# Optimization experiments

Measured on AMD Instinct MI355X. Metric: run time of the kernel, lower is better.

The kernel has to match this reference:

```python
import jax, jax.numpy as jnp
import numpy as np

NEG_SLOPE = 0.01  # torch nn.LeakyReLU default


def setup_inputs() -> dict:
    key = jax.random.key(0)
    k1, k2, k3 = jax.random.split(key, 3)
    B, H, D, L = 4, 8, 64, 2048
    q = jax.random.normal(k1, (B, H, D, L), dtype=jnp.float32)
    k = jax.random.normal(k2, (B, H, D, L), dtype=jnp.float32)
    v = jax.random.normal(k3, (B, H, D, L), dtype=jnp.float32)
    return {"q": q, "k": k, "v": v}


def reference(q, k, v):
    # q, k, v: [B, H, D, L] (note: feature dim BEFORE length, as in the torch module)
    d_tensor = q.shape[2]
    scale = 1.0 / np.sqrt(d_tensor).astype(np.float32)
    # scores = LeakyReLU(q^T k / sqrt(d)) : [B, H, Lq, Lk]
    scores = jnp.einsum('bhdq,bhdk->bhqk', q, k) * scale
    scores = jax.nn.leaky_relu(scores, negative_slope=NEG_SLOPE)
    psi = jax.nn.softmax(scores, axis=-1)
    # out = (psi @ v^T)^T : [B, H, D, Lq]
    out = jnp.einsum('bhqk,bhdk->bhdq', psi, v)
    return out
```

## Files before the change

kernel.cpp:

```cpp
#include <hip/hip_runtime.h>
#include <math.h>

#define DD 64
#define LL 2048
#define TQ 128
#define TK 64
#define NT 512
#define SCALE_LOG2 (0.125f * 1.44269504088896340736f)

typedef __bf16 bf16_t;
typedef __bf16 bf16x8 __attribute__((ext_vector_type(8)));
typedef __bf16 bf16x4 __attribute__((ext_vector_type(4)));
typedef float f32x4 __attribute__((ext_vector_type(4)));

union __align__(16) SMem {
  struct {
    bf16_t Qs[TQ][72];
    bf16_t Ks[TK][72];
    bf16_t Vs[DD][72];
    bf16_t Ps[TQ][72];
  } a;
  float Oe[TQ][65];
};

__device__ __forceinline__ unsigned pack_bf16(float lo, float hi) {
  union { bf16_t b[2]; unsigned u; } p;
  p.b[0] = (bf16_t)lo; p.b[1] = (bf16_t)hi;
  return p.u;
}

__global__ __launch_bounds__(512, 4)
void attn_flash_bf16(const float* __restrict__ q, const float* __restrict__ k,
                     const float* __restrict__ v, float* __restrict__ out) {
  __shared__ SMem sm;
  const int tid  = threadIdx.x;
  const int w    = tid >> 6;
  const int lane = tid & 63;
  const int qu   = lane >> 4;
  const int c    = lane & 15;
  const int head = blockIdx.y;
  const int q0   = blockIdx.x * TQ;
  const size_t hoff = (size_t)head * DD * LL;
  const float* qp = q + hoff;
  const float* kp = k + hoff;
  const float* vp = v + hoff;

  for (int i = 0; i < 2; ++i) {
    int idx = tid + NT * i;
    int d2  = idx >> 5;
    int c4  = (idx & 31) * 4;
    float4 qa = *(const float4*)(qp + (2 * d2) * LL + q0 + c4);
    float4 qb = *(const float4*)(qp + (2 * d2 + 1) * LL + q0 + c4);
    *(unsigned*)&sm.a.Qs[c4 + 0][2 * d2] = pack_bf16(qa.x, qb.x);
    *(unsigned*)&sm.a.Qs[c4 + 1][2 * d2] = pack_bf16(qa.y, qb.y);
    *(unsigned*)&sm.a.Qs[c4 + 2][2 * d2] = pack_bf16(qa.z, qb.z);
    *(unsigned*)&sm.a.Qs[c4 + 3][2 * d2] = pack_bf16(qa.w, qb.w);
  }
  __syncthreads();

  bf16x8 aq[2];
  aq[0] = *(const bf16x8*)&sm.a.Qs[w * 16 + c][qu * 8];
  aq[1] = *(const bf16x8*)&sm.a.Qs[w * 16 + c][32 + qu * 8];

  f32x4 oacc[4];
  float rsum[4] = {0.f, 0.f, 0.f, 0.f};
  for (int nt = 0; nt < 4; ++nt)
    for (int j = 0; j < 4; ++j) oacc[nt][j] = 0.f;

  for (int t = 0; t < LL / TK; ++t) {
    const int lk0 = t * TK;
    __syncthreads();
    {
      int d2 = tid >> 4;
      int c4 = (tid & 15) * 4;
      float4 ka = *(const float4*)(kp + (2 * d2) * LL + lk0 + c4);
      float4 kb = *(const float4*)(kp + (2 * d2 + 1) * LL + lk0 + c4);
      *(unsigned*)&sm.a.Ks[c4 + 0][2 * d2] = pack_bf16(ka.x, kb.x);
      *(unsigned*)&sm.a.Ks[c4 + 1][2 * d2] = pack_bf16(ka.y, kb.y);
      *(unsigned*)&sm.a.Ks[c4 + 2][2 * d2] = pack_bf16(ka.z, kb.z);
      *(unsigned*)&sm.a.Ks[c4 + 3][2 * d2] = pack_bf16(ka.w, kb.w);
    }
    for (int i = 0; i < 2; ++i) {
      int idx = tid + NT * i;
      int d   = idx >> 4;
      int c4  = (idx & 15) * 4;
      float4 vv = *(const float4*)(vp + d * LL + lk0 + c4);
      bf16x4 pk;
      pk[0] = (bf16_t)vv.x; pk[1] = (bf16_t)vv.y;
      pk[2] = (bf16_t)vv.z; pk[3] = (bf16_t)vv.w;
      *(bf16x4*)&sm.a.Vs[d][c4] = pk;
    }
    __syncthreads();

    f32x4 sacc[4];
    for (int nt = 0; nt < 4; ++nt)
      for (int j = 0; j < 4; ++j) sacc[nt][j] = 0.f;
    for (int kk = 0; kk < 2; ++kk)
      for (int nt = 0; nt < 4; ++nt) {
        bf16x8 bk = *(const bf16x8*)&sm.a.Ks[nt * 16 + c][kk * 32 + qu * 8];
        sacc[nt] = __builtin_amdgcn_mfma_f32_16x16x32_bf16(aq[kk], bk, sacc[nt], 0, 0, 0);
      }

    for (int r = 0; r < 4; ++r) {
      const int lq = w * 16 + qu * 4 + r;
      for (int nt = 0; nt < 4; ++nt) {
        float s = sacc[nt][r] * SCALE_LOG2;
        s = fmaxf(s, 0.01f * s);
        float p = __builtin_amdgcn_exp2f(s);
        rsum[r] += p;
        sm.a.Ps[lq][nt * 16 + c] = (bf16_t)p;
      }
    }

    for (int kk = 0; kk < 2; ++kk) {
      bf16x8 ap = *(const bf16x8*)&sm.a.Ps[w * 16 + c][kk * 32 + qu * 8];
      for (int nt = 0; nt < 4; ++nt) {
        bf16x8 bv = *(const bf16x8*)&sm.a.Vs[nt * 16 + c][kk * 32 + qu * 8];
        oacc[nt] = __builtin_amdgcn_mfma_f32_16x16x32_bf16(ap, bv, oacc[nt], 0, 0, 0);
      }
    }
  }

  for (int r = 0; r < 4; ++r) {
    float rs = rsum[r];
    rs += __shfl_xor(rs, 1);
    rs += __shfl_xor(rs, 2);
    rs += __shfl_xor(rs, 4);
    rs += __shfl_xor(rs, 8);
    rsum[r] = 1.0f / rs;
  }

  __syncthreads();
  for (int r = 0; r < 4; ++r) {
    const int lq = w * 16 + qu * 4 + r;
    for (int nt = 0; nt < 4; ++nt)
      sm.Oe[lq][nt * 16 + c] = oacc[nt][r] * rsum[r];
  }
  __syncthreads();
  float* op = out + hoff + q0;
  for (int i = 0; i < 16; ++i) {
    int idx = tid + NT * i;
    int d   = idx >> 7;
    int lq  = idx & 127;
    op[d * LL + lq] = sm.Oe[lq][d];
  }
}

extern "C" void kernel_launch(void* const* d_in, const int* in_sizes, int n_in,
                              void* d_out, int out_size, void* d_ws, size_t ws_size,
                              hipStream_t stream) {
  const float* q = (const float*)d_in[0];
  const float* k = (const float*)d_in[1];
  const float* v = (const float*)d_in[2];
  float* out = (float*)d_out;
  dim3 grid(LL / TQ, 32);
  attn_flash_bf16<<<grid, 512, 0, stream>>>(q, k, v, out);
}
```

Baseline: 165.2 us.

## Switch to 32x32 MFMA with transposed scores so P stays in registers

The score tile is now computed transposed with 32x32x16 bf16 MFMAs, K as the A operand and Q as the B operand. Each lane therefore owns one query column, and the probabilities can be repacked into PV A-operands with cross-half-wave shuffles instead of a round trip through shared memory. The softmax scale and log2e are folded into Q at load time. The block shrinks to 256 threads with four waves of 32 query rows each, and the P buffer is removed from shared memory. The cost is more register pressure from 16-element accumulators, plus scalar strided global loads for Q and K in place of float4 loads.

```diff
diff --git a/kernel.cpp b/kernel.cpp
--- a/kernel.cpp
+++ b/kernel.cpp
@@ -5,39 +5,34 @@
 #define LL 2048
 #define TQ 128
 #define TK 64
-#define NT 512
-#define SCALE_LOG2 (0.125f * 1.44269504088896340736f)
+#define NT 256
+#define QSCALE 0.18033688011112042f
 
 typedef __bf16 bf16_t;
 typedef __bf16 bf16x8 __attribute__((ext_vector_type(8)));
 typedef __bf16 bf16x4 __attribute__((ext_vector_type(4)));
-typedef float f32x4 __attribute__((ext_vector_type(4)));
+typedef float f32x16 __attribute__((ext_vector_type(16)));
 
-union __align__(16) SMem {
-  struct {
-    bf16_t Qs[TQ][72];
-    bf16_t Ks[TK][72];
-    bf16_t Vs[DD][72];
-    bf16_t Ps[TQ][72];
-  } a;
+struct __align__(16) SMemA {
+  bf16_t Qs[TQ][72];
+  bf16_t Ks[TK][72];
+  bf16_t Vs[DD][72];
+};
+union __align__(16) SMemU {
+  SMemA a;
   float Oe[TQ][65];
 };
 
-__device__ __forceinline__ unsigned pack_bf16(float lo, float hi) {
-  union { bf16_t b[2]; unsigned u; } p;
-  p.b[0] = (bf16_t)lo; p.b[1] = (bf16_t)hi;
-  return p.u;
-}
-
-__global__ __launch_bounds__(512, 4)
+__global__ __launch_bounds__(256, 2)
 void attn_flash_bf16(const float* __restrict__ q, const float* __restrict__ k,
                      const float* __restrict__ v, float* __restrict__ out) {
-  __shared__ SMem sm;
+  __shared__ SMemU sm;
+  __shared__ float rs[TQ];
   const int tid  = threadIdx.x;
   const int w    = tid >> 6;
   const int lane = tid & 63;
-  const int qu   = lane >> 4;
-  const int c    = lane & 15;
+  const int l31  = lane & 31;
+  const int hh   = lane >> 5;
   const int head = blockIdx.y;
   const int q0   = blockIdx.x * TQ;
   const size_t hoff = (size_t)head * DD * LL;
@@ -45,46 +40,48 @@
   const float* kp = k + hoff;
   const float* vp = v + hoff;
 
-  for (int i = 0; i < 2; ++i) {
-    int idx = tid + NT * i;
-    int d2  = idx >> 5;
-    int c4  = (idx & 31) * 4;
-    float4 qa = *(const float4*)(qp + (2 * d2) * LL + q0 + c4);
-    float4 qb = *(const float4*)(qp + (2 * d2 + 1) * LL + q0 + c4);
-    *(unsigned*)&sm.a.Qs[c4 + 0][2 * d2] = pack_bf16(qa.x, qb.x);
-    *(unsigned*)&sm.a.Qs[c4 + 1][2 * d2] = pack_bf16(qa.y, qb.y);
-    *(unsigned*)&sm.a.Qs[c4 + 2][2 * d2] = pack_bf16(qa.z, qb.z);
-    *(unsigned*)&sm.a.Qs[c4 + 3][2 * d2] = pack_bf16(qa.w, qb.w);
+  {
+    int lq = tid & 127;
+    int d0 = (tid >> 7) * 32;
+    const float* src = qp + q0 + lq;
+    for (int g = 0; g < 4; ++g) {
+      bf16x8 pk;
+      for (int j = 0; j < 8; ++j)
+        pk[j] = (bf16_t)(src[(size_t)(d0 + g * 8 + j) * LL] * QSCALE);
+      *(bf16x8*)&sm.a.Qs[lq][d0 + g * 8] = pk;
+    }
   }
   __syncthreads();
 
-  bf16x8 aq[2];
-  aq[0] = *(const bf16x8*)&sm.a.Qs[w * 16 + c][qu * 8];
-  aq[1] = *(const bf16x8*)&sm.a.Qs[w * 16 + c][32 + qu * 8];
+  const int wbase = w * 32;
+  bf16x8 bq[4];
+  for (int kk = 0; kk < 4; ++kk)
+    bq[kk] = *(const bf16x8*)&sm.a.Qs[wbase + l31][kk * 16 + 8 * hh];
 
-  f32x4 oacc[4];
-  float rsum[4] = {0.f, 0.f, 0.f, 0.f};
-  for (int nt = 0; nt < 4; ++nt)
-    for (int j = 0; j < 4; ++j) oacc[nt][j] = 0.f;
+  f32x16 oacc[2];
+  for (int dt = 0; dt < 2; ++dt)
+    for (int r = 0; r < 16; ++r) oacc[dt][r] = 0.f;
+  float rsum = 0.f;
 
   for (int t = 0; t < LL / TK; ++t) {
     const int lk0 = t * TK;
     __syncthreads();
     {
-      int d2 = tid >> 4;
-      int c4 = (tid & 15) * 4;
-      float4 ka = *(const float4*)(kp + (2 * d2) * LL + lk0 + c4);
-      float4 kb = *(const float4*)(kp + (2 * d2 + 1) * LL + lk0 + c4);
-      *(unsigned*)&sm.a.Ks[c4 + 0][2 * d2] = pack_bf16(ka.x, kb.x);
-      *(unsigned*)&sm.a.Ks[c4 + 1][2 * d2] = pack_bf16(ka.y, kb.y);
-      *(unsigned*)&sm.a.Ks[c4 + 2][2 * d2] = pack_bf16(ka.z, kb.z);
-      *(unsigned*)&sm.a.Ks[c4 + 3][2 * d2] = pack_bf16(ka.w, kb.w);
+      int lk = tid & 63;
+      int d0 = (tid >> 6) * 16;
+      const float* src = kp + lk0 + lk;
+      for (int g = 0; g < 2; ++g) {
+        bf16x8 pk;
+        for (int j = 0; j < 8; ++j)
+          pk[j] = (bf16_t)src[(size_t)(d0 + g * 8 + j) * LL];
+        *(bf16x8*)&sm.a.Ks[lk][d0 + g * 8] = pk;
+      }
     }
-    for (int i = 0; i < 2; ++i) {
+    for (int i = 0; i < 4; ++i) {
       int idx = tid + NT * i;
       int d   = idx >> 4;
       int c4  = (idx & 15) * 4;
-      float4 vv = *(const float4*)(vp + d * LL + lk0 + c4);
+      float4 vv = *(const float4*)(vp + (size_t)d * LL + lk0 + c4);
       bf16x4 pk;
       pk[0] = (bf16_t)vv.x; pk[1] = (bf16_t)vv.y;
       pk[2] = (bf16_t)vv.z; pk[3] = (bf16_t)vv.w;
@@ -92,57 +89,73 @@
     }
     __syncthreads();
 
-    f32x4 sacc[4];
-    for (int nt = 0; nt < 4; ++nt)
-      for (int j = 0; j < 4; ++j) sacc[nt][j] = 0.f;
-    for (int kk = 0; kk < 2; ++kk)
-      for (int nt = 0; nt < 4; ++nt) {
-        bf16x8 bk = *(const bf16x8*)&sm.a.Ks[nt * 16 + c][kk * 32 + qu * 8];
-        sacc[nt] = __builtin_amdgcn_mfma_f32_16x16x32_bf16(aq[kk], bk, sacc[nt], 0, 0, 0);
+    f32x16 st[2];
+    for (int nt = 0; nt < 2; ++nt)
+      for (int r = 0; r < 16; ++r) st[nt][r] = 0.f;
+    for (int nt = 0; nt < 2; ++nt)
+      for (int kk = 0; kk < 4; ++kk) {
+        bf16x8 ak = *(const bf16x8*)&sm.a.Ks[nt * 32 + l31][kk * 16 + 8 * hh];
+        st[nt] = __builtin_amdgcn_mfma_f32_32x32x16_bf16(ak, bq[kk], st[nt], 0, 0, 0);
       }
 
-    for (int r = 0; r < 4; ++r) {
-      const int lq = w * 16 + qu * 4 + r;
-      for (int nt = 0; nt < 4; ++nt) {
-        float s = sacc[nt][r] * SCALE_LOG2;
+    unsigned pb[2][8];
+    for (int nt = 0; nt < 2; ++nt) {
+      for (int r = 0; r < 16; ++r) {
+        float s = st[nt][r];
         s = fmaxf(s, 0.01f * s);
         float p = __builtin_amdgcn_exp2f(s);
-        rsum[r] += p;
-        sm.a.Ps[lq][nt * 16 + c] = (bf16_t)p;
+        rsum += p;
+        st[nt][r] = p;
+      }
+      for (int qq = 0; qq < 8; ++qq) {
+        union { bf16_t b[2]; unsigned u; } pk;
+        pk.b[0] = (bf16_t)st[nt][2 * qq];
+        pk.b[1] = (bf16_t)st[nt][2 * qq + 1];
+        pb[nt][qq] = pk.u;
       }
     }
 
-    for (int kk = 0; kk < 2; ++kk) {
-      bf16x8 ap = *(const bf16x8*)&sm.a.Ps[w * 16 + c][kk * 32 + qu * 8];
-      for (int nt = 0; nt < 4; ++nt) {
-        bf16x8 bv = *(const bf16x8*)&sm.a.Vs[nt * 16 + c][kk * 32 + qu * 8];
-        oacc[nt] = __builtin_amdgcn_mfma_f32_16x16x32_bf16(ap, bv, oacc[nt], 0, 0, 0);
+    for (int nt = 0; nt < 2; ++nt)
+      for (int kk2 = 0; kk2 < 2; ++kk2) {
+        unsigned l0 = pb[nt][4 * kk2 + 0], l1 = pb[nt][4 * kk2 + 1];
+        unsigned l2 = pb[nt][4 * kk2 + 2], l3 = pb[nt][4 * kk2 + 3];
+        unsigned s0 = hh ? l0 : l2;
+        unsigned s1 = hh ? l1 : l3;
+        unsigned f0 = (unsigned)__shfl_xor((int)s0, 32);
+        unsigned f1 = (unsigned)__shfl_xor((int)s1, 32);
+        union { unsigned u[4]; bf16x8 v; } ap;
+        ap.u[0] = hh ? f0 : l0;
+        ap.u[1] = hh ? f1 : l1;
+        ap.u[2] = hh ? l2 : f0;
+        ap.u[3] = hh ? l3 : f1;
+        const int lkb = nt * 32 + kk2 * 16 + 8 * hh;
+        for (int dt = 0; dt < 2; ++dt) {
+          bf16x8 bv = *(const bf16x8*)&sm.a.Vs[dt * 32 + l31][lkb];
+          oacc[dt] = __builtin_amdgcn_mfma_f32_32x32x16_bf16(ap.v, bv, oacc[dt], 0, 0, 0);
+        }
       }
-    }
   }
 
-  for (int r = 0; r < 4; ++r) {
-    float rs = rsum[r];
-    rs += __shfl_xor(rs, 1);
-    rs += __shfl_xor(rs, 2);
-    rs += __shfl_xor(rs, 4);
-    rs += __shfl_xor(rs, 8);
-    rsum[r] = 1.0f / rs;
+  float rtot = rsum + __shfl_xor(rsum, 32);
+  rs[wbase + l31] = 1.0f / rtot;
+  float inv[16];
+  for (int r = 0; r < 16; ++r) {
+    int row = (r & 3) + 8 * (r >> 2) + 4 * hh;
+    inv[r] = rs[wbase + row];
   }
-
   __syncthreads();
-  for (int r = 0; r < 4; ++r) {
-    const int lq = w * 16 + qu * 4 + r;
-    for (int nt = 0; nt < 4; ++nt)
-      sm.Oe[lq][nt * 16 + c] = oacc[nt][r] * rsum[r];
+  for (int r = 0; r < 16; ++r) {
+    int row = (r & 3) + 8 * (r >> 2) + 4 * hh;
+    for (int dt = 0; dt < 2; ++dt)
+      sm.Oe[wbase + row][dt * 32 + l31] = oacc[dt][r] * inv[r];
   }
   __syncthreads();
   float* op = out + hoff + q0;
-  for (int i = 0; i < 16; ++i) {
+  for (int i = 0; i < 32; ++i) {
     int idx = tid + NT * i;
     int d   = idx >> 7;
     int lq  = idx & 127;
-    op[d * LL + lq] = sm.Oe[lq][d];
+    op[(size_t)d * LL + lq] = sm.Oe[lq][d];
   }
 }
 
@@ -154,5 +167,5 @@
   const float* v = (const float*)d_in[2];
   float* out = (float*)d_out;
   dim3 grid(LL / TQ, 32);
-  attn_flash_bf16<<<grid, 512, 0, stream>>>(q, k, v, out);
+  attn_flash_bf16<<<grid, 256, 0, stream>>>(q, k, v, out);
 }
```

Result: slower. 209.6 us (+26.9%).
